# Kernel tuning notes

Measured on AMD Instinct MI355X. Metric: run time of the kernel, lower is better.

Reference implementation:

```python
import jax, jax.numpy as jnp
import numpy as np

B=1; NW=8; SEG=511; S=NW*(SEG+1); W=256; C=S//W; H=12; D=64; DM=768; FF=3072; V=50265; L=12; OUT=128; G=NW
SCALE = float(1.0/np.sqrt(D))
GPOS = np.arange(NW)*(S//NW)                      # global (CLS) token positions
IDX = np.arange(C)[:,None]*W + np.arange(3*W)[None,:]   # [C,3W] gather into padded key seq
_band = np.abs(np.arange(3*W)[None,:]-np.arange(W)[:,None]-W) <= W   # [W,3W] |rel|<=W band
_kpos = IDX - W
LMASK = _band[None] & ((_kpos>=0)&(_kpos<S))[:,None,:]  # [C,W,3W]

def _ln(x, s, b):
    m = jnp.mean(x, -1, keepdims=True)
    v = jnp.mean((x-m)**2, -1, keepdims=True)
    return (x-m)*jax.lax.rsqrt(v+1e-5)*s + b

def _layer(h, Wq,bq,Wk,bk,Wv,bv,Wo,bo,Wqg,bqg,Wkg,bkg,Wvg,bvg,l1s,l1b,W1,b1,W2,b2,l2s,l2b):
    hd = lambda z: z.reshape(B,S,H,D).transpose(0,2,1,3)   # [B,H,S,D]
    q = hd(h@Wq+bq)*SCALE
    k = hd(h@Wk+bk); v = hd(h@Wv+bv)
    kc = jnp.pad(k, ((0,0),(0,0),(W,W),(0,0)))[:,:,IDX]    # [B,H,C,3W,D]
    vc = jnp.pad(v, ((0,0),(0,0),(W,W),(0,0)))[:,:,IDX]
    qc = q.reshape(B,H,C,W,D)
    # banded local scores + scores to global keys, joint softmax (HF longformer style)
    sl = jnp.where(LMASK, jnp.einsum('bhcqd,bhckd->bhcqk', qc, kc), -1e9)
    sg = jnp.einsum('bhcqd,bhgd->bhcqg', qc, k[:,:,GPOS])
    a = jax.nn.softmax(jnp.concatenate([sg, sl], -1), -1)  # [B,H,C,W,G+3W]
    out = jnp.einsum('bhcqg,bhgd->bhcqd', a[..., :G], v[:,:,GPOS]) \
        + jnp.einsum('bhcqk,bhckd->bhcqd', a[..., G:], vc)
    out = out.reshape(B,H,S,D)
    # global tokens: full attention with separate global projections, overwrite their outputs
    qg = (h[:,GPOS]@Wqg+bqg).reshape(B,G,H,D).transpose(0,2,1,3)*SCALE
    ag = jax.nn.softmax(jnp.einsum('bhgd,bhsd->bhgs', qg, hd(h@Wkg+bkg)), -1)
    out = out.at[:,:,GPOS,:].set(jnp.einsum('bhgs,bhsd->bhgd', ag, hd(h@Wvg+bvg)))
    y = out.transpose(0,2,1,3).reshape(B,S,DM)@Wo + bo
    h = _ln(h + y, l1s, l1b)
    return _ln(h + jax.nn.gelu(h@W1+b1)@W2 + b2, l2s, l2b)

def setup_inputs() -> dict:
    keys = iter(jax.random.split(jax.random.key(0), 64))
    p = lambda *s: jax.random.normal(next(keys), s, jnp.float32)*0.02
    d = {"x": jax.random.randint(next(keys), (B, NW*SEG), 0, V),
         "word_emb": p(V, DM), "pos_emb": p(S, DM),
         "emb_ln_s": jnp.ones((DM,)), "emb_ln_b": jnp.zeros((DM,))}
    for n in ["Wq","Wk","Wv","Wo","Wqg","Wkg","Wvg"]:
        d[n] = p(L, DM, DM); d["b"+n[1:]] = jnp.zeros((L, DM))
    d["ln1_s"]=jnp.ones((L,DM)); d["ln1_b"]=jnp.zeros((L,DM))
    d["W1"]=p(L,DM,FF); d["b1"]=jnp.zeros((L,FF))
    d["W2"]=p(L,FF,DM); d["b2"]=jnp.zeros((L,DM))
    d["ln2_s"]=jnp.ones((L,DM)); d["ln2_b"]=jnp.zeros((L,DM))
    d["Wout"]=p(DM,OUT); d["bout"]=jnp.zeros((OUT,))
    return d

def reference(x, word_emb, pos_emb, emb_ln_s, emb_ln_b, Wq, bq, Wk, bk, Wv, bv, Wo, bo,
              Wqg, bqg, Wkg, bkg, Wvg, bvg, ln1_s, ln1_b, W1, b1, W2, b2, ln2_s, ln2_b,
              Wout, bout):
    # prepend CLS (id 0) per window -> S=4096 token ids
    ids = jnp.concatenate([jnp.zeros((B, NW, 1), x.dtype), x.reshape(B, NW, SEG)], 2).reshape(B, S)
    h = _ln(word_emb[ids] + pos_emb[None], emb_ln_s, emb_ln_b)
    for l in range(L):
        h = _layer(h, Wq[l],bq[l],Wk[l],bk[l],Wv[l],bv[l],Wo[l],bo[l],
                   Wqg[l],bqg[l],Wkg[l],bkg[l],Wvg[l],bvg[l],
                   ln1_s[l],ln1_b[l],W1[l],b1[l],W2[l],b2[l],ln2_s[l],ln2_b[l])
    return h[:, GPOS] @ Wout + bout   # cls_pooling + output head: [B, NW, OUT]
```

## Files before the change

kernel.cpp:

```cpp
#include <hip/hip_runtime.h>
#include <hip/hip_bf16.h>


typedef unsigned short u16;
typedef __attribute__((ext_vector_type(4))) float floatx4;
typedef __attribute__((ext_vector_type(4))) unsigned int uintx4;
typedef __attribute__((ext_vector_type(8))) short bf16x8;
typedef __attribute__((ext_vector_type(4))) u16 u16x4;

#define S_LEN 4096
#define QKVG_N 4608
#define NL 12

__device__ inline u16 f2bf(float x) {
    union { __hip_bfloat16 b; u16 u; } cv;
    cv.b = __float2bfloat16(x);
    return cv.u;
}
__device__ inline float bf2f(u16 u) {
    union { float f; unsigned int i; } c; c.i = ((unsigned int)u) << 16; return c.f;
}
__device__ inline float gelu_f(float x) {
    float x3 = x * x * x;
    return 0.5f * x * (1.0f + tanhf(0.7978845608028654f * (x + 0.044715f * x3)));
}

#define GLDS16(g, l)                                                              \
    __builtin_amdgcn_global_load_lds(                                             \
        (const __attribute__((address_space(1))) unsigned int*)(g),               \
        (__attribute__((address_space(3))) unsigned int*)(l), 16, 0, 0)

__global__ __launch_bounds__(256) void prep_weights_k(
    const float* __restrict__ Wq0, const float* __restrict__ Wk0, const float* __restrict__ Wv0,
    const float* __restrict__ Wkg0, const float* __restrict__ Wvg0, const float* __restrict__ Wqg0,
    const float* __restrict__ Wo0, const float* __restrict__ W10, const float* __restrict__ W20,
    const float* __restrict__ bq0, const float* __restrict__ bk0, const float* __restrict__ bv0,
    const float* __restrict__ bkg0, const float* __restrict__ bvg0, const float* __restrict__ bqg0,
    u16* __restrict__ wTall, float* __restrict__ bcatall)
{
    const int l = blockIdx.y;
    const size_t sqo = (size_t)l * 589824;
    const size_t sff = (size_t)l * 2359296;
    u16* wqkvgT = wTall + (size_t)l * 8847360;
    u16* woT = wqkvgT + 3538944;
    u16* w1T = woT + 589824;
    u16* w2T = w1T + 2359296;

    int bid = blockIdx.x;
    int t = threadIdx.x;
    if (bid >= 2160) {
        int i = (bid - 2160) * 256 + t;
        float v;
        if (i < 768)       v = bq0[l * 768 + i];
        else if (i < 1536) v = bk0[l * 768 + i - 768];
        else if (i < 2304) v = bv0[l * 768 + i - 1536];
        else if (i < 3072) v = bkg0[l * 768 + i - 2304];
        else if (i < 3840) v = bvg0[l * 768 + i - 3072];
        else               v = bqg0[l * 768 + i - 3840];
        bcatall[(size_t)l * 4608 + i] = v;
        return;
    }
    const float* src; u16* dst; int K, N, tile;
    if (bid < 864) {
        int m = bid / 144; tile = bid % 144;
        src = ((m == 0) ? Wq0 : (m == 1) ? Wk0 : (m == 2) ? Wv0 :
               (m == 3) ? Wkg0 : (m == 4) ? Wvg0 : Wqg0) + sqo;
        dst = wqkvgT + (size_t)m * 589824;
        K = 768; N = 768;
    } else if (bid < 1008) { tile = bid - 864;  src = Wo0 + sqo; dst = woT; K = 768;  N = 768; }
    else if (bid < 1584)   { tile = bid - 1008; src = W10 + sff; dst = w1T; K = 768;  N = 3072; }
    else                   { tile = bid - 1584; src = W20 + sff; dst = w2T; K = 3072; N = 768; }

    int nt = N >> 6;
    int k0 = (tile / nt) << 6, n0 = (tile % nt) << 6;
    __shared__ float tb[64][65];
    int r = t >> 4, c4 = (t & 15) * 4;
    #pragma unroll
    for (int j = 0; j < 4; j++) {
        int kk = r + j * 16;
        floatx4 v = *(const floatx4*)&src[(size_t)(k0 + kk) * N + n0 + c4];
        #pragma unroll
        for (int i = 0; i < 4; i++) tb[c4 + i][kk] = v[i];
    }
    __syncthreads();
    int k4 = (t & 15) * 4, nb = t >> 4;
    #pragma unroll
    for (int j = 0; j < 4; j++) {
        int n = nb + j * 16;
        u16x4 o;
        #pragma unroll
        for (int i = 0; i < 4; i++) o[i] = f2bf(tb[n][k4 + i]);
        *(u16x4*)&dst[(size_t)(n0 + n) * K + k0 + k4] = o;
    }
}

template <int ACT, int WF, int WB, int SKIPQG, int WVT, int SPLITB>
__global__ __launch_bounds__(256, 3) void gemm_k(
    const u16* __restrict__ A, const u16* __restrict__ Bt,
    const float* __restrict__ bias,
    float* __restrict__ Cf, u16* __restrict__ Cb, u16* __restrict__ vTg,
    int N, int K, int lda, int ldb)
{
    int lin = blockIdx.y * 32 + blockIdx.x;
    int qq = gridDim.y << 2;
    int wg = (lin & 7) * qq + (lin >> 3);
    int bx = wg & 31, by = wg >> 5;
    if (SKIPQG && by >= 30 && (bx & 3) != 0) return;
    int bm = bx * 128, bn = by * 128;
    const int zoff = SPLITB ? blockIdx.z : 0;
    const u16* Ab = A + (size_t)zoff * K;
    const u16* Bb = Bt + (size_t)zoff * K;
    float* Cfz = WF ? Cf + (size_t)zoff * S_LEN * N : (float*)nullptr;

    __shared__ __align__(16) u16 As[128][64];
    __shared__ __align__(16) u16 Bs[128][64];
    int t = threadIdx.x, lane = t & 63, wv = t >> 6;
    int wm = (wv >> 1) * 64, wn = (wv & 1) * 64;
    int srow = t >> 3, scol = (t & 7) * 8;
    int fr = lane & 15, fo = (lane >> 4) * 8;

    floatx4 acc[4][4];
    #pragma unroll
    for (int i = 0; i < 4; i++)
        #pragma unroll
        for (int j = 0; j < 4; j++) acc[i][j] = (floatx4){0.f, 0.f, 0.f, 0.f};

    const int nk = K >> 6;
    for (int kt = 0; kt < nk; ++kt) {
        const u16* ag = Ab + (size_t)(bm + srow) * lda + kt * 64 + scol;
        const u16* bg = Bb + (size_t)(bn + srow) * ldb + kt * 64 + scol;
        #pragma unroll
        for (int c = 0; c < 4; ++c) {
            GLDS16(ag + (size_t)(32 * c) * lda, &As[srow + 32 * c][scol]);
            GLDS16(bg + (size_t)(32 * c) * ldb, &Bs[srow + 32 * c][scol]);
        }
        __syncthreads();
        #pragma unroll
        for (int ks = 0; ks < 2; ++ks) {
            bf16x8 af[4], bfr[4];
            #pragma unroll
            for (int i = 0; i < 4; i++) af[i]  = *(const bf16x8*)&As[wm + i * 16 + fr][ks * 32 + fo];
            #pragma unroll
            for (int i = 0; i < 4; i++) bfr[i] = *(const bf16x8*)&Bs[wn + i * 16 + fr][ks * 32 + fo];
            #pragma unroll
            for (int i = 0; i < 4; i++)
                #pragma unroll
                for (int j = 0; j < 4; j++)
                    acc[i][j] = __builtin_amdgcn_mfma_f32_16x16x32_bf16(af[i], bfr[j], acc[i][j], 0, 0, 0);
        }
        __syncthreads();
    }

    int dr = (lane >> 4) * 4, dc = lane & 15;
    #pragma unroll
    for (int i = 0; i < 4; i++) {
        #pragma unroll
        for (int j = 0; j < 4; j++) {
            int r0 = bm + wm + i * 16 + dr;
            int cc = bn + wn + j * 16 + dc;
            float bsv = (!SPLITB || blockIdx.z == 0) ? bias[cc] : 0.f;
            u16x4 tv;
            #pragma unroll
            for (int r = 0; r < 4; r++) {
                float v = acc[i][j][r] + bsv;
                if (ACT == 1) v = gelu_f(v);
                if (WF) Cfz[(size_t)(r0 + r) * N + cc] = v;
                if (WB) { u16 b = f2bf(v); Cb[(size_t)(r0 + r) * N + cc] = b; tv[r] = b; }
            }
            if (WVT && cc >= 1536 && cc < 2304)
                *(u16x4*)&vTg[(size_t)(cc - 1536) * 4096 + r0] = tv;
        }
    }
}

__global__ __launch_bounds__(256) void attn_local_k(
    const u16* __restrict__ qkvg, const u16* __restrict__ vTg, u16* __restrict__ aob)
{
    int lin = blockIdx.y * 64 + blockIdx.x;
    int wg = (lin & 7) * 96 + (lin >> 3);
    const int qb = wg & 63, hh = wg >> 6;
    const int t = threadIdx.x, lane = t & 63, w = t >> 6;
    const int g = lane >> 4, qi = lane & 15;
    __shared__ __align__(16) u16 ks[64][72];
    __shared__ __align__(16) u16 vt[64][72];
    __shared__ __align__(16) u16 pbuf[4][16][40];

    const int q0w = qb * 64 + w * 16;
    const int sq = q0w + qi;

    bf16x8 qf0, qf1;
    {
        const u16* qp = qkvg + (size_t)(q0w + qi) * QKVG_N + hh * 64 + g * 8;
        qf0 = *(const bf16x8*)qp;
        qf1 = *(const bf16x8*)(qp + 32);
    }

    floatx4 acc[4];
    #pragma unroll
    for (int i = 0; i < 4; i++) acc[i] = (floatx4){0.f, 0.f, 0.f, 0.f};
    float mrun = -1e30f, lrun = 0.f;

    for (int tile = 0; tile <= 9; ++tile) {
        const int kbase = qb * 64 - 256 + (tile - 1) * 64;
        if (tile > 0 && (kbase < 0 || kbase >= S_LEN)) continue;
        __syncthreads();
        if (tile == 0) {
            for (int i = t; i < 576; i += 256) ((uintx4*)vt)[i] = (uintx4){0, 0, 0, 0};
            __syncthreads();
            if (t < 64) {
                int gg = t >> 3, d0 = (t & 7) * 8;
                *(uintx4*)&ks[gg][d0] =
                    *(const uintx4*)(qkvg + (size_t)(gg * 512) * QKVG_N + 768 + hh * 64 + d0);
            }
            for (int e = t; e < 512; e += 256) {
                int d = e >> 3, gg = e & 7;
                vt[d][gg] = vTg[(size_t)(hh * 64 + d) * 4096 + gg * 512];
            }
        } else {
            for (int c = t; c < 512; c += 256) {
                int r = c >> 3, c0 = (c & 7) * 8;
                *(uintx4*)&ks[r][c0] =
                    *(const uintx4*)(qkvg + (size_t)(kbase + r) * QKVG_N + 768 + hh * 64 + c0);
                *(uintx4*)&vt[r][c0] =
                    *(const uintx4*)(vTg + (size_t)(hh * 64 + r) * 4096 + kbase + c0);
            }
        }
        __syncthreads();

        const bool gt = (tile == 0);
        const bool edge = (tile == 1) | (tile == 9);
        const int ng = gt ? 1 : 2;
        for (int kg2 = 0; kg2 < ng; ++kg2) {
            floatx4 sf[2];
            sf[1] = (floatx4){0.f, 0.f, 0.f, 0.f};
            {
                bf16x8 ka0 = *(const bf16x8*)&ks[kg2 * 32 + qi][g * 8];
                bf16x8 ka1 = *(const bf16x8*)&ks[kg2 * 32 + qi][32 + g * 8];
                floatx4 z = (floatx4){0.f, 0.f, 0.f, 0.f};
                z = __builtin_amdgcn_mfma_f32_16x16x32_bf16(ka0, qf0, z, 0, 0, 0);
                sf[0] = __builtin_amdgcn_mfma_f32_16x16x32_bf16(ka1, qf1, z, 0, 0, 0);
            }
            if (!gt) {
                bf16x8 kb0 = *(const bf16x8*)&ks[kg2 * 32 + 16 + qi][g * 8];
                bf16x8 kb1 = *(const bf16x8*)&ks[kg2 * 32 + 16 + qi][32 + g * 8];
                floatx4 z = (floatx4){0.f, 0.f, 0.f, 0.f};
                z = __builtin_amdgcn_mfma_f32_16x16x32_bf16(kb0, qf0, z, 0, 0, 0);
                sf[1] = __builtin_amdgcn_mfma_f32_16x16x32_bf16(kb1, qf1, z, 0, 0, 0);
            }
            float p8[8];
            float mloc = -1e30f;
            #pragma unroll
            for (int f = 0; f < 2; ++f)
                #pragma unroll
                for (int r = 0; r < 4; ++r) {
                    int kl = kg2 * 32 + f * 16 + g * 4 + r;
                    float sc = sf[f][r] * 0.125f;
                    if (gt) {
                        if (kl >= 8) sc = -1e30f;
                    } else if (edge) {
                        int dd = kbase + kl - sq;
                        if (dd > 256 || dd < -256) sc = -1e30f;
                    }
                    p8[f * 4 + r] = sc;
                    mloc = fmaxf(mloc, sc);
                }
            mloc = fmaxf(mloc, __shfl_xor(mloc, 16));
            mloc = fmaxf(mloc, __shfl_xor(mloc, 32));
            float mnew = fmaxf(mrun, mloc);
            float alpha = __expf(mrun - mnew);
            mrun = mnew;
            float ls = 0.f;
            #pragma unroll
            for (int i = 0; i < 8; ++i) { float p = __expf(p8[i] - mnew); p8[i] = p; ls += p; }
            ls += __shfl_xor(ls, 16);
            ls += __shfl_xor(ls, 32);
            lrun = lrun * alpha + ls;
            u16x4 w0, w1;
            #pragma unroll
            for (int r = 0; r < 4; ++r) { w0[r] = f2bf(p8[r]); w1[r] = f2bf(p8[4 + r]); }
            *(u16x4*)&pbuf[w][qi][g * 4] = w0;
            *(u16x4*)&pbuf[w][qi][16 + g * 4] = w1;
            float al[4];
            #pragma unroll
            for (int r = 0; r < 4; ++r) al[r] = __shfl(alpha, g * 4 + r);
            #pragma unroll
            for (int dt = 0; dt < 4; ++dt)
                #pragma unroll
                for (int r = 0; r < 4; ++r) acc[dt][r] *= al[r];
            bf16x8 pf = *(const bf16x8*)&pbuf[w][qi][g * 8];
            #pragma unroll
            for (int dt = 0; dt < 4; ++dt) {
                bf16x8 vb = *(const bf16x8*)&vt[dt * 16 + qi][kg2 * 32 + g * 8];
                acc[dt] = __builtin_amdgcn_mfma_f32_16x16x32_bf16(pf, vb, acc[dt], 0, 0, 0);
            }
        }
    }

    float inv = 1.f / lrun;
    float li[4];
    #pragma unroll
    for (int r = 0; r < 4; ++r) li[r] = __shfl(inv, g * 4 + r);
    #pragma unroll
    for (int dt = 0; dt < 4; ++dt)
        #pragma unroll
        for (int r = 0; r < 4; ++r) {
            int s = q0w + g * 4 + r;
            aob[(size_t)s * 768 + hh * 64 + dt * 16 + qi] = f2bf(acc[dt][r] * li[r]);
        }
}

#define BLOCK_MEANVAR(sum, sq, mean, inv)                                        \
    {                                                                            \
        for (int o_ = 32; o_ > 0; o_ >>= 1) {                                    \
            sum += __shfl_down(sum, o_); sq += __shfl_down(sq, o_);              \
        }                                                                        \
        __shared__ float rs_[4], rq_[4];                                         \
        if ((threadIdx.x & 63) == 0) { rs_[threadIdx.x >> 6] = sum; rq_[threadIdx.x >> 6] = sq; } \
        __syncthreads();                                                         \
        float S_ = rs_[0] + rs_[1] + rs_[2] + rs_[3];                            \
        float Q_ = rq_[0] + rq_[1] + rq_[2] + rq_[3];                            \
        mean = S_ * (1.f / 768.f);                                               \
        float var_ = Q_ * (1.f / 768.f) - mean * mean;                           \
        inv = rsqrtf(var_ + 1e-5f);                                              \
    }

__global__ __launch_bounds__(256) void embed_ln_k(
    const int* __restrict__ x, const float* __restrict__ wemb, const float* __restrict__ pemb,
    const float* __restrict__ gs, const float* __restrict__ gb,
    float* __restrict__ hf, u16* __restrict__ hb)
{
    int s = blockIdx.x, t = threadIdx.x;
    int w = s >> 9, p = s & 511;
    int id = (p == 0) ? 0 : x[w * 511 + p - 1];
    float v[3], sum = 0.f, sq = 0.f;
    #pragma unroll
    for (int r = 0; r < 3; r++) {
        int d = t + r * 256;
        float e = wemb[(size_t)id * 768 + d] + pemb[(size_t)s * 768 + d];
        v[r] = e; sum += e; sq += e * e;
    }
    float mean, inv;
    BLOCK_MEANVAR(sum, sq, mean, inv)
    #pragma unroll
    for (int r = 0; r < 3; r++) {
        int d = t + r * 256;
        float y = (v[r] - mean) * inv * gs[d] + gb[d];
        hf[(size_t)s * 768 + d] = y;
        hb[(size_t)s * 768 + d] = f2bf(y);
    }
}

__global__ __launch_bounds__(192) void ln_resid_k(
    const float* __restrict__ xa, const float* __restrict__ xb, const float* __restrict__ xc,
    const float* __restrict__ gs, const float* __restrict__ gb,
    float* __restrict__ of, u16* __restrict__ ob)
{
    int s = blockIdx.x, t = threadIdx.x;
    floatx4 a = *(const floatx4*)(xa + (size_t)s * 768 + t * 4);
    floatx4 b = *(const floatx4*)(xb + (size_t)s * 768 + t * 4);
    floatx4 c = *(const floatx4*)(xc + (size_t)s * 768 + t * 4);
    floatx4 v;
    #pragma unroll
    for (int i = 0; i < 4; i++) v[i] = a[i] + b[i] + c[i];
    float sum = v[0] + v[1] + v[2] + v[3];
    float sq = v[0] * v[0] + v[1] * v[1] + v[2] * v[2] + v[3] * v[3];
    #pragma unroll
    for (int o = 32; o > 0; o >>= 1) {
        sum += __shfl_down(sum, o); sq += __shfl_down(sq, o);
    }
    __shared__ float rs_[3], rq_[3];
    if ((t & 63) == 0) { rs_[t >> 6] = sum; rq_[t >> 6] = sq; }
    __syncthreads();
    float S = rs_[0] + rs_[1] + rs_[2];
    float Q = rq_[0] + rq_[1] + rq_[2];
    float mean = S * (1.f / 768.f);
    float inv = rsqrtf(Q * (1.f / 768.f) - mean * mean + 1e-5f);
    floatx4 g4 = *(const floatx4*)(gs + t * 4);
    floatx4 b4 = *(const floatx4*)(gb + t * 4);
    floatx4 y;
    u16x4 o4;
    #pragma unroll
    for (int i = 0; i < 4; i++) {
        y[i] = (v[i] - mean) * inv * g4[i] + b4[i];
        o4[i] = f2bf(y[i]);
    }
    *(floatx4*)(of + (size_t)s * 768 + t * 4) = y;
    *(u16x4*)(ob + (size_t)s * 768 + t * 4) = o4;
}

__global__ __launch_bounds__(256) void attn_gpart_k(
    const u16* __restrict__ qkvg,
    float* __restrict__ pacc, float* __restrict__ pm, float* __restrict__ pl)
{
    const int hh = blockIdx.x, ck = blockIdx.y;
    const int t = threadIdx.x;
    __shared__ float qs[8][64];
    __shared__ __align__(16) u16 ks[128][72];
    __shared__ __align__(16) u16 vs[128][64];
    __shared__ float sc[8][128];
    __shared__ float mred[8], lred[8];

    for (int i = t; i < 512; i += 256) {
        int g = i >> 6, d = i & 63;
        qs[g][d] = bf2f(qkvg[(size_t)(g * 512) * QKVG_N + 3840 + hh * 64 + d]) * 0.125f;
    }
    const int s0 = ck * 128;
    for (int u = t; u < 1024; u += 256) {
        int r = u >> 3, c = u & 7;
        const u16* src = qkvg + (size_t)(s0 + r) * QKVG_N + hh * 64 + c * 8;
        *(uintx4*)&ks[r][c * 8] = *(const uintx4*)(src + 2304);
        *(uintx4*)&vs[r][c * 8] = *(const uintx4*)(src + 3072);
    }
    __syncthreads();

    {
        int key = t & 127, q0 = (t >> 7) * 4;
        float a[4] = {0.f, 0.f, 0.f, 0.f};
        #pragma unroll
        for (int c = 0; c < 8; ++c) {
            uintx4 pk = *(const uintx4*)&ks[key][c * 8];
            const u16* uu = (const u16*)&pk;
            #pragma unroll
            for (int e = 0; e < 8; ++e) {
                float kv = bf2f(uu[e]);
                #pragma unroll
                for (int q = 0; q < 4; ++q) a[q] += kv * qs[q0 + q][c * 8 + e];
            }
        }
        #pragma unroll
        for (int q = 0; q < 4; ++q) sc[q0 + q][key] = a[q];
    }
    __syncthreads();

    {
        int q = t >> 5, lq = t & 31;
        float m = -1e30f;
        #pragma unroll
        for (int i = 0; i < 4; ++i) m = fmaxf(m, sc[q][lq + i * 32]);
        #pragma unroll
        for (int o = 1; o < 32; o <<= 1) m = fmaxf(m, __shfl_xor(m, o));
        float ls = 0.f;
        #pragma unroll
        for (int i = 0; i < 4; ++i) {
            float p = __expf(sc[q][lq + i * 32] - m);
            sc[q][lq + i * 32] = p; ls += p;
        }
        #pragma unroll
        for (int o = 1; o < 32; o <<= 1) ls += __shfl_xor(ls, o);
        if (lq == 0) { mred[q] = m; lred[q] = ls; }
    }
    __syncthreads();

    {
        int d = t & 63, qb = t >> 6;
        float a0 = 0.f, a1 = 0.f;
        #pragma unroll 4
        for (int s = 0; s < 128; ++s) {
            float v = bf2f(vs[s][d]);
            a0 += sc[qb][s] * v;
            a1 += sc[qb + 4][s] * v;
        }
        float* pb = pacc + (((size_t)hh * 32 + ck) * 8) * 64;
        pb[qb * 64 + d] = a0;
        pb[(qb + 4) * 64 + d] = a1;
        if (t < 8) {
            pm[((size_t)hh * 32 + ck) * 8 + t] = mred[t];
            pl[((size_t)hh * 32 + ck) * 8 + t] = lred[t];
        }
    }
}

__global__ __launch_bounds__(64) void attn_gred_k(
    const float* __restrict__ pacc, const float* __restrict__ pm,
    const float* __restrict__ pl, u16* __restrict__ aob)
{
    int hh = blockIdx.x, gq = blockIdx.y;
    int d = threadIdx.x;
    float M = -1e30f;
    #pragma unroll 4
    for (int c = 0; c < 32; ++c)
        M = fmaxf(M, pm[((size_t)hh * 32 + c) * 8 + gq]);
    float L = 0.f, o = 0.f;
    #pragma unroll 4
    for (int c = 0; c < 32; ++c) {
        float w = __expf(pm[((size_t)hh * 32 + c) * 8 + gq] - M);
        L += pl[((size_t)hh * 32 + c) * 8 + gq] * w;
        o += w * pacc[(((size_t)hh * 32 + c) * 8 + gq) * 64 + d];
    }
    aob[(size_t)(gq * 512) * 768 + hh * 64 + d] = f2bf(o / L);
}

__global__ __launch_bounds__(128) void head_k(
    const float* __restrict__ hf, const float* __restrict__ Wout,
    const float* __restrict__ bout, float* __restrict__ out)
{
    int g = blockIdx.x, n = threadIdx.x;
    __shared__ float hsh[768];
    for (int i = n; i < 768; i += 128) hsh[i] = hf[(size_t)(g * 512) * 768 + i];
    __syncthreads();
    float a = 0.f;
    #pragma unroll 4
    for (int k = 0; k < 768; k++) a += hsh[k] * Wout[k * 128 + n];
    out[g * 128 + n] = a + bout[n];
}

extern "C" void kernel_launch(void* const* d_in, const int* in_sizes, int n_in,
                              void* d_out, int out_size, void* d_ws, size_t ws_size,
                              hipStream_t stream)
{
    (void)in_sizes; (void)n_in; (void)out_size; (void)ws_size;
    const int*   x    = (const int*)  d_in[0];
    const float* wemb = (const float*)d_in[1];
    const float* pemb = (const float*)d_in[2];
    const float* elns = (const float*)d_in[3];
    const float* elnb = (const float*)d_in[4];
    const float* Wq   = (const float*)d_in[5];
    const float* bq   = (const float*)d_in[6];
    const float* Wk   = (const float*)d_in[7];
    const float* bk   = (const float*)d_in[8];
    const float* Wv   = (const float*)d_in[9];
    const float* bv   = (const float*)d_in[10];
    const float* Wo   = (const float*)d_in[11];
    const float* bo   = (const float*)d_in[12];
    const float* Wqg  = (const float*)d_in[13];
    const float* bqg  = (const float*)d_in[14];
    const float* Wkg  = (const float*)d_in[15];
    const float* bkg  = (const float*)d_in[16];
    const float* Wvg  = (const float*)d_in[17];
    const float* bvg  = (const float*)d_in[18];
    const float* l1s  = (const float*)d_in[19];
    const float* l1b  = (const float*)d_in[20];
    const float* W1   = (const float*)d_in[21];
    const float* b1   = (const float*)d_in[22];
    const float* W2   = (const float*)d_in[23];
    const float* b2   = (const float*)d_in[24];
    const float* l2s  = (const float*)d_in[25];
    const float* l2b  = (const float*)d_in[26];
    const float* Wout = (const float*)d_in[27];
    const float* boutp= (const float*)d_in[28];

    char* W = (char*)d_ws;
    float* hf    = (float*)(W);
    u16*   hb    = (u16*)  (W + 12582912);
    u16*   qkvg  = (u16*)  (W + 18874368);
    u16*   vTg   = (u16*)  (W + 56623104);
    u16*   aob   = (u16*)  (W + 62914560);
    float* yf    = (float*)(W + 69206016);
    u16*   ff1b  = (u16*)  (W + 94371840);
    float* pacc  = (float*)(W + 119537664);
    float* pmw   = (float*)(W + 120324096);
    float* plw   = (float*)(W + 120336384);
    float* bcatall = (float*)(W + 120348672);
    u16*   wTall = (u16*)  (W + 120569856);

    prep_weights_k<<<dim3(2178, 12), 256, 0, stream>>>(
        Wq, Wk, Wv, Wkg, Wvg, Wqg, Wo, W1, W2,
        bq, bk, bv, bkg, bvg, bqg, wTall, bcatall);

    embed_ln_k<<<4096, 256, 0, stream>>>(x, wemb, pemb, elns, elnb, hf, hb);

    float* yf0 = yf;
    float* yf1 = yf + (size_t)4096 * 768;

    for (int l = 0; l < NL; ++l) {
        u16* wTl      = wTall + (size_t)l * 8847360;
        u16* wqkvgT_l = wTl;
        u16* woT_l    = wTl + 3538944;
        u16* w1T_l    = woT_l + 589824;
        u16* w2T_l    = w1T_l + 2359296;
        float* bcat_l = bcatall + (size_t)l * 4608;
        const float* bo_l  = bo  + (size_t)l * 768;
        const float* b1_l  = b1  + (size_t)l * 3072;
        const float* b2_l  = b2  + (size_t)l * 768;
        const float* l1s_l = l1s + (size_t)l * 768;
        const float* l1b_l = l1b + (size_t)l * 768;
        const float* l2s_l = l2s + (size_t)l * 768;
        const float* l2b_l = l2b + (size_t)l * 768;

        gemm_k<0, 0, 1, 1, 1, 0><<<dim3(32, 36), 256, 0, stream>>>(
            hb, wqkvgT_l, bcat_l, (float*)nullptr, qkvg, vTg, QKVG_N, 768, 768, 768);

        attn_local_k<<<dim3(64, 12), 256, 0, stream>>>(qkvg, vTg, aob);

        attn_gpart_k<<<dim3(12, 32), 256, 0, stream>>>(qkvg, pacc, pmw, plw);
        attn_gred_k<<<dim3(12, 8), 64, 0, stream>>>(pacc, pmw, plw, aob);

        gemm_k<0, 1, 0, 0, 0, 1><<<dim3(32, 6, 2), 256, 0, stream>>>(
            aob, woT_l, bo_l, yf, (u16*)nullptr, (u16*)nullptr, 768, 384, 768, 768);
        ln_resid_k<<<4096, 192, 0, stream>>>(hf, yf0, yf1, l1s_l, l1b_l, hf, hb);

        gemm_k<1, 0, 1, 0, 0, 0><<<dim3(32, 24), 256, 0, stream>>>(
            hb, w1T_l, b1_l, (float*)nullptr, ff1b, (u16*)nullptr, 3072, 768, 768, 768);
        gemm_k<0, 1, 0, 0, 0, 1><<<dim3(32, 6, 2), 256, 0, stream>>>(
            ff1b, w2T_l, b2_l, yf, (u16*)nullptr, (u16*)nullptr, 768, 1536, 3072, 3072);
        ln_resid_k<<<4096, 192, 0, stream>>>(hf, yf0, yf1, l2s_l, l2b_l, hf, hb);
    }

    head_k<<<8, 128, 0, stream>>>(hf, Wout, boutp, (float*)d_out);
}
```

Before: 2.893 ms.

## Split-K four ways for Wo/W2 GEMMs, restructure weight prep, alias ff1b buffer

The Wo and W2 GEMMs now split K four ways instead of two, giving 768 blocks rather than 384 so more CUs are busy. ln_resid sums the four fp32 partials itself. The weight-prep kernel becomes a 1D grid where each block transposes four 64x64 tiles, with register prefetch and a double-buffered LDS tile. ff1b now shares memory with the qkvg buffer. The cost is more partial-sum traffic, since yf grows to four slabs, plus extra reads in the LayerNorm.

```diff
diff --git a/kernel.cpp b/kernel.cpp
--- a/kernel.cpp
+++ b/kernel.cpp
@@ -38,59 +38,77 @@
     const float* __restrict__ bkg0, const float* __restrict__ bvg0, const float* __restrict__ bqg0,
     u16* __restrict__ wTall, float* __restrict__ bcatall)
 {
-    const int l = blockIdx.y;
+    const int t = threadIdx.x;
+    const int bid = blockIdx.x;
+    if (bid >= 6480) {
+        int i = (bid - 6480) * 256 + t;
+        int l = i / 4608, j = i - l * 4608;
+        float v;
+        if (j < 768)       v = bq0[l * 768 + j];
+        else if (j < 1536) v = bk0[l * 768 + j - 768];
+        else if (j < 2304) v = bv0[l * 768 + j - 1536];
+        else if (j < 3072) v = bkg0[l * 768 + j - 2304];
+        else if (j < 3840) v = bvg0[l * 768 + j - 3072];
+        else               v = bqg0[l * 768 + j - 3840];
+        bcatall[(size_t)l * 4608 + j] = v;
+        return;
+    }
+
+    const int l = bid / 540, b = bid - l * 540;
     const size_t sqo = (size_t)l * 589824;
     const size_t sff = (size_t)l * 2359296;
-    u16* wqkvgT = wTall + (size_t)l * 8847360;
-    u16* woT = wqkvgT + 3538944;
-    u16* w1T = woT + 589824;
-    u16* w2T = w1T + 2359296;
-
-    int bid = blockIdx.x;
-    int t = threadIdx.x;
-    if (bid >= 2160) {
-        int i = (bid - 2160) * 256 + t;
-        float v;
-        if (i < 768)       v = bq0[l * 768 + i];
-        else if (i < 1536) v = bk0[l * 768 + i - 768];
-        else if (i < 2304) v = bv0[l * 768 + i - 1536];
-        else if (i < 3072) v = bkg0[l * 768 + i - 2304];
-        else if (i < 3840) v = bvg0[l * 768 + i - 3072];
-        else               v = bqg0[l * 768 + i - 3840];
-        bcatall[(size_t)l * 4608 + i] = v;
-        return;
-    }
-    const float* src; u16* dst; int K, N, tile;
-    if (bid < 864) {
-        int m = bid / 144; tile = bid % 144;
+    u16* wq = wTall + (size_t)l * 8847360;
+    const float* src; u16* dst; int K, N, kt, ns;
+    if (b < 216) {
+        int m = b / 36, s = b - m * 36;
         src = ((m == 0) ? Wq0 : (m == 1) ? Wk0 : (m == 2) ? Wv0 :
                (m == 3) ? Wkg0 : (m == 4) ? Wvg0 : Wqg0) + sqo;
-        dst = wqkvgT + (size_t)m * 589824;
-        K = 768; N = 768;
-    } else if (bid < 1008) { tile = bid - 864;  src = Wo0 + sqo; dst = woT; K = 768;  N = 768; }
-    else if (bid < 1584)   { tile = bid - 1008; src = W10 + sff; dst = w1T; K = 768;  N = 3072; }
-    else                   { tile = bid - 1584; src = W20 + sff; dst = w2T; K = 3072; N = 768; }
-
-    int nt = N >> 6;
-    int k0 = (tile / nt) << 6, n0 = (tile % nt) << 6;
-    __shared__ float tb[64][65];
-    int r = t >> 4, c4 = (t & 15) * 4;
-    #pragma unroll
-    for (int j = 0; j < 4; j++) {
-        int kk = r + j * 16;
-        floatx4 v = *(const floatx4*)&src[(size_t)(k0 + kk) * N + n0 + c4];
-        #pragma unroll
-        for (int i = 0; i < 4; i++) tb[c4 + i][kk] = v[i];
-    }
-    __syncthreads();
-    int k4 = (t & 15) * 4, nb = t >> 4;
-    #pragma unroll
-    for (int j = 0; j < 4; j++) {
-        int n = nb + j * 16;
-        u16x4 o;
-        #pragma unroll
-        for (int i = 0; i < 4; i++) o[i] = f2bf(tb[n][k4 + i]);
-        *(u16x4*)&dst[(size_t)(n0 + n) * K + k0 + k4] = o;
+        dst = wq + (size_t)m * 589824;
+        K = 768; N = 768; kt = s / 3; ns = s - kt * 3;
+    } else if (b < 252) {
+        int s = b - 216; src = Wo0 + sqo; dst = wq + 3538944;
+        K = 768; N = 768; kt = s / 3; ns = s - kt * 3;
+    } else if (b < 396) {
+        int s = b - 252; src = W10 + sff; dst = wq + 4128768;
+        K = 768; N = 3072; kt = s / 12; ns = s - kt * 12;
+    } else {
+        int s = b - 396; src = W20 + sff; dst = wq + 6488064;
+        K = 3072; N = 768; kt = s / 3; ns = s - kt * 3;
+    }
+    const int k0 = kt * 64, n0b = ns * 256;
+
+    __shared__ float tb[2][64][65];
+    const int r = t >> 4, c4 = (t & 15) * 4;
+    const float* srow = src + (size_t)k0 * N + n0b;
+    floatx4 rg[4];
+    #pragma unroll
+    for (int j = 0; j < 4; j++)
+        rg[j] = *(const floatx4*)&srow[(size_t)(r + 16 * j) * N + c4];
+
+    #pragma unroll
+    for (int s4 = 0; s4 < 4; ++s4) {
+        float (*tbb)[65] = tb[s4 & 1];
+        #pragma unroll
+        for (int j = 0; j < 4; j++) {
+            int kk = r + 16 * j;
+            #pragma unroll
+            for (int i = 0; i < 4; i++) tbb[c4 + i][kk] = rg[j][i];
+        }
+        __syncthreads();
+        if (s4 < 3) {
+            #pragma unroll
+            for (int j = 0; j < 4; j++)
+                rg[j] = *(const floatx4*)&srow[(size_t)(r + 16 * j) * N + (s4 + 1) * 64 + c4];
+        }
+        int n0 = n0b + s4 * 64;
+        #pragma unroll
+        for (int j = 0; j < 4; j++) {
+            int n = r + 16 * j;
+            u16x4 o;
+            #pragma unroll
+            for (int i = 0; i < 4; i++) o[i] = f2bf(tbb[n][c4 + i]);
+            *(u16x4*)&dst[(size_t)(n0 + n) * K + k0 + c4] = o;
+        }
     }
 }
 
@@ -351,17 +369,19 @@
 }
 
 __global__ __launch_bounds__(192) void ln_resid_k(
-    const float* __restrict__ xa, const float* __restrict__ xb, const float* __restrict__ xc,
+    const float* __restrict__ xa, const float* __restrict__ yf,
     const float* __restrict__ gs, const float* __restrict__ gb,
     float* __restrict__ of, u16* __restrict__ ob)
 {
     int s = blockIdx.x, t = threadIdx.x;
-    floatx4 a = *(const floatx4*)(xa + (size_t)s * 768 + t * 4);
-    floatx4 b = *(const floatx4*)(xb + (size_t)s * 768 + t * 4);
-    floatx4 c = *(const floatx4*)(xc + (size_t)s * 768 + t * 4);
-    floatx4 v;
-    #pragma unroll
-    for (int i = 0; i < 4; i++) v[i] = a[i] + b[i] + c[i];
+    size_t off = (size_t)s * 768 + t * 4;
+    floatx4 v = *(const floatx4*)(xa + off);
+    #pragma unroll
+    for (int z = 0; z < 4; z++) {
+        floatx4 b = *(const floatx4*)(yf + (size_t)z * 4096 * 768 + off);
+        #pragma unroll
+        for (int i = 0; i < 4; i++) v[i] += b[i];
+    }
     float sum = v[0] + v[1] + v[2] + v[3];
     float sq = v[0] * v[0] + v[1] * v[1] + v[2] * v[2] + v[3] * v[3];
     #pragma unroll
@@ -384,8 +404,8 @@
         y[i] = (v[i] - mean) * inv * g4[i] + b4[i];
         o4[i] = f2bf(y[i]);
     }
-    *(floatx4*)(of + (size_t)s * 768 + t * 4) = y;
-    *(u16x4*)(ob + (size_t)s * 768 + t * 4) = o4;
+    *(floatx4*)(of + off) = y;
+    *(u16x4*)(ob + off) = o4;
 }
 
 __global__ __launch_bounds__(256) void attn_gpart_k(
@@ -543,24 +563,21 @@
     float* hf    = (float*)(W);
     u16*   hb    = (u16*)  (W + 12582912);
     u16*   qkvg  = (u16*)  (W + 18874368);
+    u16*   ff1b  = (u16*)  (W + 18874368);
     u16*   vTg   = (u16*)  (W + 56623104);
     u16*   aob   = (u16*)  (W + 62914560);
     float* yf    = (float*)(W + 69206016);
-    u16*   ff1b  = (u16*)  (W + 94371840);
     float* pacc  = (float*)(W + 119537664);
     float* pmw   = (float*)(W + 120324096);
     float* plw   = (float*)(W + 120336384);
     float* bcatall = (float*)(W + 120348672);
     u16*   wTall = (u16*)  (W + 120569856);
 
-    prep_weights_k<<<dim3(2178, 12), 256, 0, stream>>>(
+    prep_weights_k<<<6696, 256, 0, stream>>>(
         Wq, Wk, Wv, Wkg, Wvg, Wqg, Wo, W1, W2,
         bq, bk, bv, bkg, bvg, bqg, wTall, bcatall);
 
     embed_ln_k<<<4096, 256, 0, stream>>>(x, wemb, pemb, elns, elnb, hf, hb);
-
-    float* yf0 = yf;
-    float* yf1 = yf + (size_t)4096 * 768;
 
     for (int l = 0; l < NL; ++l) {
         u16* wTl      = wTall + (size_t)l * 8847360;
@@ -585,15 +602,15 @@
         attn_gpart_k<<<dim3(12, 32), 256, 0, stream>>>(qkvg, pacc, pmw, plw);
         attn_gred_k<<<dim3(12, 8), 64, 0, stream>>>(pacc, pmw, plw, aob);
 
-        gemm_k<0, 1, 0, 0, 0, 1><<<dim3(32, 6, 2), 256, 0, stream>>>(
-            aob, woT_l, bo_l, yf, (u16*)nullptr, (u16*)nullptr, 768, 384, 768, 768);
-        ln_resid_k<<<4096, 192, 0, stream>>>(hf, yf0, yf1, l1s_l, l1b_l, hf, hb);
+        gemm_k<0, 1, 0, 0, 0, 1><<<dim3(32, 6, 4), 256, 0, stream>>>(
+            aob, woT_l, bo_l, yf, (u16*)nullptr, (u16*)nullptr, 768, 192, 768, 768);
+        ln_resid_k<<<4096, 192, 0, stream>>>(hf, yf, l1s_l, l1b_l, hf, hb);
 
         gemm_k<1, 0, 1, 0, 0, 0><<<dim3(32, 24), 256, 0, stream>>>(
             hb, w1T_l, b1_l, (float*)nullptr, ff1b, (u16*)nullptr, 3072, 768, 768, 768);
-        gemm_k<0, 1, 0, 0, 0, 1><<<dim3(32, 6, 2), 256, 0, stream>>>(
-            ff1b, w2T_l, b2_l, yf, (u16*)nullptr, (u16*)nullptr, 768, 1536, 3072, 3072);
-        ln_resid_k<<<4096, 192, 0, stream>>>(hf, yf0, yf1, l2s_l, l2b_l, hf, hb);
+        gemm_k<0, 1, 0, 0, 0, 1><<<dim3(32, 6, 4), 256, 0, stream>>>(
+            ff1b, w2T_l, b2_l, yf, (u16*)nullptr, (u16*)nullptr, 768, 768, 3072, 3072);
+        ln_resid_k<<<4096, 192, 0, stream>>>(hf, yf, l2s_l, l2b_l, hf, hb);
     }
 
     head_k<<<8, 128, 0, stream>>>(hf, Wout, boutp, (float*)d_out);
```

After: 2.838 ms. About the same (-1.9%).
